# Performance work log

Measured on AMD Instinct MI355X. Metric: run time of the kernel, lower is better.

## Reference

```python
import jax, jax.numpy as jnp
import numpy as np

N, E = 50000, 800000
IN_DIM, HID, OUT = 512, 128, 64
EPS = 0.3
N_LAYERS = 2


def setup_inputs() -> dict:
    key = jax.random.key(0)
    ks = jax.random.split(key, 10)
    src = jax.random.randint(ks[0], (E,), 0, N, dtype=jnp.int32)
    dst = jax.random.randint(ks[1], (E,), 0, N, dtype=jnp.int32)
    yes_no = jax.random.randint(ks[2], (E,), 0, 2, dtype=jnp.int32)
    # symmetric degree norm d = (deg+1)^-1/2 (self-loop-adjusted, as in DGL FAGCN)
    deg = jax.ops.segment_sum(jnp.ones((E,), jnp.float32), dst, num_segments=N)
    d = jax.lax.rsqrt(deg + 1.0)
    return {
        "h": jax.random.normal(ks[3], (N, IN_DIM), jnp.float32),
        "d": d,
        "t1_w": jax.random.normal(ks[4], (HID, IN_DIM), jnp.float32) * (1.414 / np.sqrt(IN_DIM)),
        "t1_b": jnp.zeros((HID,), jnp.float32),
        "gate_w": jax.random.normal(ks[5], (N_LAYERS, 2 * HID), jnp.float32) * (1.414 / np.sqrt(2 * HID)),
        "gate_b": jnp.zeros((N_LAYERS,), jnp.float32),
        "t2_w": jax.random.normal(ks[6], (OUT, HID), jnp.float32) * (1.414 / np.sqrt(HID)),
        "t2_b": jnp.zeros((OUT,), jnp.float32),
        "yes_weight": jnp.float32(1.5),
        "no_weight": jnp.float32(-0.5),
        "src": src,
        "dst": dst,
        "yes_no": yes_no,
    }


def reference(h, d, t1_w, t1_b, gate_w, gate_b, t2_w, t2_b, yes_weight, no_weight, src, dst, yes_no):
    n = h.shape[0]
    hdim = t1_w.shape[0]
    yn = yes_no.astype(h.dtype)
    # yes/no edge bias is layer-independent
    yn_term = jnp.tanh(yn * yes_weight + (1.0 - yn) * no_weight)  # [E]
    dd = d[dst] * d[src]  # [E]

    x = jax.nn.relu(h @ t1_w.T + t1_b)  # [N, H] (dropout is identity in eval)
    raw = x
    for i in range(gate_w.shape[0]):
        # gate(concat(h_dst, h_src)) == h@w_dst (gathered at dst) + h@w_src (gathered at src)
        gd = x @ gate_w[i, :hdim]   # [N]
        gs = x @ gate_w[i, hdim:]   # [N]
        g = jnp.tanh(gd[dst] + gs[src] + gate_b[i])  # [E]
        e = (g + yn_term) * 0.5 * dd                 # [E]
        msg = x[src] * e[:, None]                    # [E, H]
        z = jax.ops.segment_sum(msg, dst, num_segments=n)  # [N, H]
        x = EPS * raw + z
    logits = x @ t2_w.T + t2_b
    return jax.nn.log_softmax(logits, axis=1)
```

## Files before the change

kernel.cpp:

```cpp
#include <hip/hip_runtime.h>
#include <math.h>

#define N_NODES 50000
#define N_EDGES 800000
#define IN_DIM  512
#define HID     128
#define OUT_DIM 64
#define EPS     0.3f

#define SCAN_BLOCKS 49
#define LDS_ROW 516

typedef __attribute__((ext_vector_type(8))) short bf16x8;
typedef __attribute__((ext_vector_type(8))) __bf16 bf16v8;
typedef __attribute__((ext_vector_type(4))) float f32x4;

__device__ __forceinline__ float fast_tanh(float x) {
    return 1.0f - 2.0f / (__expf(2.0f * x) + 1.0f);
}

__device__ __forceinline__ unsigned short f2bfu(float f) {
    return __builtin_bit_cast(unsigned short, (__bf16)f);
}
__device__ __forceinline__ unsigned pk2(float lo, float hi) {
    return (unsigned)f2bfu(lo) | ((unsigned)f2bfu(hi) << 16);
}
__device__ __forceinline__ float bf_lo(unsigned u) { return __uint_as_float(u << 16); }
__device__ __forceinline__ float bf_hi(unsigned u) { return __uint_as_float(u & 0xffff0000u); }

__device__ __forceinline__ int deg_of(float dv) {
    return (int)(1.0f / (dv * dv) + 0.5f) - 1;
}


__global__ void hw_k(const float* __restrict__ d, int* __restrict__ partials,
                     const float* __restrict__ w, unsigned short* __restrict__ wb) {
    int bid = blockIdx.x, tid = threadIdx.x;

    if (bid < SCAN_BLOCKS) {
        int base = bid * 1024 + tid * 4;
        int s = 0;
#pragma unroll
        for (int j = 0; j < 4; j++) if (base + j < N_NODES) s += deg_of(d[base + j]);
#pragma unroll
        for (int off = 32; off; off >>= 1) s += __shfl_down(s, off);
        __shared__ int ws[4];
        int lane = tid & 63, wv = tid >> 6;
        if (lane == 0) ws[wv] = s;
        __syncthreads();
        if (tid == 0) partials[bid] = ws[0] + ws[1] + ws[2] + ws[3];
        return;
    }

    int t = (bid - SCAN_BLOCKS) * 256 + tid;
    int lane = t & 63;
    int ct   = (t >> 6) & 7;
    int ks   = t >> 9;
    int row  = ct * 16 + (lane & 15);
    int kb   = ks * 32 + (lane >> 4) * 8;
    const float* p = &w[(size_t)row * IN_DIM + kb];
    float4 v0 = *(const float4*)p, v1 = *(const float4*)(p + 4);
    uint4 pk;
    pk.x = pk2(v0.x, v0.y);
    pk.y = pk2(v0.z, v0.w);
    pk.z = pk2(v1.x, v1.y);
    pk.w = pk2(v1.z, v1.w);
    *(uint4*)&wb[(size_t)t * 8] = pk;
}


__global__ void scanw_k(const float* __restrict__ d, const int* __restrict__ partials,
                        int* __restrict__ rowptr, int* __restrict__ cursor) {
    int tid = threadIdx.x;
    int base = blockIdx.x * 1024 + tid * 4;
    int v[4]; int s = 0;
#pragma unroll
    for (int j = 0; j < 4; j++) {
        v[j] = (base + j < N_NODES) ? deg_of(d[base + j]) : 0;
        s += v[j];
    }
    int lane = tid & 63, wv = tid >> 6;
    int sc = s;
#pragma unroll
    for (int off = 1; off < 64; off <<= 1) {
        int t = __shfl_up(sc, off);
        if (lane >= off) sc += t;
    }
    __shared__ int wtot[4];
    __shared__ int bofs_s;
    if (lane == 63) wtot[wv] = sc;
    if (tid < 64) {
        int p = (tid < blockIdx.x) ? partials[tid] : 0;
#pragma unroll
        for (int off = 32; off; off >>= 1) p += __shfl_down(p, off);
        if (tid == 0) bofs_s = p;
    }
    __syncthreads();
    int wof = 0;
    for (int w = 0; w < wv; w++) wof += wtot[w];
    int excl = bofs_s + wof + (sc - s);
#pragma unroll
    for (int j = 0; j < 4; j++) {
        if (base + j < N_NODES) { rowptr[base + j] = excl; cursor[base + j] = excl; }
        excl += v[j];
    }
    if (blockIdx.x == SCAN_BLOCKS - 1 && tid == 0)
        rowptr[N_NODES] = bofs_s + wtot[0] + wtot[1] + wtot[2] + wtot[3];
}


__launch_bounds__(256)
__global__ void t1fill_k(const float* __restrict__ h, const unsigned short* __restrict__ wb,
                         const float* __restrict__ bias, const float* __restrict__ gw0,
                         unsigned short* __restrict__ xb0,
                         float* __restrict__ gd0, float* __restrict__ gs0,
                         const int* __restrict__ src, const int* __restrict__ dst,
                         const int* __restrict__ yn, int* __restrict__ cursor,
                         int* __restrict__ csr) {
    __shared__ float At[16 * LDS_ROW];
    __shared__ float red[4][4][4][2];

    if (blockIdx.x & 1) {
        int e = (blockIdx.x >> 1) * 256 + threadIdx.x;
        int dv = dst[e];
        int pos = atomicAdd(&cursor[dv], 1);
        csr[pos] = src[e] | (yn[e] << 31);
        return;
    }

    int tid  = threadIdx.x;
    int lane = tid & 63;
    int wv   = tid >> 6;
    int l15  = lane & 15;
    int quad = lane >> 4;
    int rowb = (blockIdx.x >> 1) * 16;

#pragma unroll
    for (int i = 0; i < 8; ++i) {
        int c    = wv * 8 + i;
        int row  = c >> 1, half = c & 1;
        const float* gsrc = &h[(size_t)(rowb + row) * IN_DIM + half * 256 + lane * 4];
        float* ldst = &At[row * LDS_ROW + half * 256];
        __builtin_amdgcn_global_load_lds(
            (const __attribute__((address_space(1))) unsigned int*)gsrc,
            (__attribute__((address_space(3))) unsigned int*)ldst, 16, 0, 0);
    }
    __syncthreads();

    int ct0 = wv * 2;
    const unsigned short* bp = &wb[(size_t)lane * 8];
    const float* arp = &At[l15 * LDS_ROW + quad * 8];
    f32x4 acc[2];
    acc[0] = (f32x4){0.f, 0.f, 0.f, 0.f};
    acc[1] = (f32x4){0.f, 0.f, 0.f, 0.f};
#pragma unroll 4
    for (int ks = 0; ks < 16; ++ks) {
        float4 a0 = *(const float4*)(arp + ks * 32);
        float4 a1 = *(const float4*)(arp + ks * 32 + 4);
        bf16v8 av;
        av[0] = (__bf16)a0.x; av[1] = (__bf16)a0.y;
        av[2] = (__bf16)a0.z; av[3] = (__bf16)a0.w;
        av[4] = (__bf16)a1.x; av[5] = (__bf16)a1.y;
        av[6] = (__bf16)a1.z; av[7] = (__bf16)a1.w;
        bf16x8 af = __builtin_bit_cast(bf16x8, av);
        bf16x8 b0 = *(const bf16x8*)(bp + (size_t)(ks * 8 + ct0) * 512);
        bf16x8 b1 = *(const bf16x8*)(bp + (size_t)(ks * 8 + ct0 + 1) * 512);
        acc[0] = __builtin_amdgcn_mfma_f32_16x16x32_bf16(af, b0, acc[0], 0, 0, 0);
        acc[1] = __builtin_amdgcn_mfma_f32_16x16x32_bf16(af, b1, acc[1], 0, 0, 0);
    }

    float pd[4] = {0.f, 0.f, 0.f, 0.f}, ps[4] = {0.f, 0.f, 0.f, 0.f};
#pragma unroll
    for (int ct = 0; ct < 2; ++ct) {
        int o = (ct0 + ct) * 16 + l15;
        float b = bias[o];
        float wd = gw0[o], wsv = gw0[128 + o];
#pragma unroll
        for (int r = 0; r < 4; ++r) {
            float v = acc[ct][r] + b;
            v = v > 0.f ? v : 0.f;
            int node = rowb + quad * 4 + r;
            xb0[(size_t)node * HID + o] = f2bfu(v);
            pd[r] += v * wd; ps[r] += v * wsv;
        }
    }
#pragma unroll
    for (int m = 1; m < 16; m <<= 1) {
#pragma unroll
        for (int r = 0; r < 4; ++r) {
            pd[r] += __shfl_xor(pd[r], m);
            ps[r] += __shfl_xor(ps[r], m);
        }
    }
    if (l15 == 0) {
#pragma unroll
        for (int r = 0; r < 4; ++r) {
            red[wv][quad][r][0] = pd[r];
            red[wv][quad][r][1] = ps[r];
        }
    }
    __syncthreads();
    if (wv == 0 && lane < 16) {
        int q = lane >> 2, r = lane & 3;
        float sd = red[0][q][r][0] + red[1][q][r][0] + red[2][q][r][0] + red[3][q][r][0];
        float ss = red[0][q][r][1] + red[1][q][r][1] + red[2][q][r][1] + red[3][q][r][1];
        gd0[rowb + lane] = sd;
        gs0[rowb + lane] = ss;
    }
}


__global__ void agg_k(const unsigned short* __restrict__ xb,
                      const unsigned short* __restrict__ rb,
                      const int* __restrict__ rowptr, const int* __restrict__ csr,
                      const float* __restrict__ d,
                      const float* __restrict__ gd, const float* __restrict__ gs,
                      const float* __restrict__ gb, int layer,
                      const float* __restrict__ yw, const float* __restrict__ nw,
                      const float* __restrict__ gw_next,
                      float* __restrict__ gd_out, float* __restrict__ gs_out,
                      unsigned short* __restrict__ xb_out) {
    int t = blockIdx.x * blockDim.x + threadIdx.x;
    int nid = t >> 6, lane = t & 63;
    if (nid >= N_NODES) return;
    int l15 = lane & 15, eg = lane >> 4;
    float acc[8];
#pragma unroll
    for (int j = 0; j < 8; j++) acc[j] = 0.f;
    if (lane < 16) {
        uint4 rv = *(const uint4*)&rb[(size_t)nid * HID + l15 * 8];
        acc[0] = EPS * bf_lo(rv.x); acc[1] = EPS * bf_hi(rv.x);
        acc[2] = EPS * bf_lo(rv.y); acc[3] = EPS * bf_hi(rv.y);
        acc[4] = EPS * bf_lo(rv.z); acc[5] = EPS * bf_hi(rv.z);
        acc[6] = EPS * bf_lo(rv.w); acc[7] = EPS * bf_hi(rv.w);
    }
    float gdn = gd[nid] + gb[layer];
    float dn  = d[nid];
    float ty  = fast_tanh(yw[0]);
    float tno = fast_tanh(nw[0]);
    int e0 = rowptr[nid], e1 = rowptr[nid + 1];
    for (int b0 = e0; b0 < e1; b0 += 64) {
        int e = b0 + lane;
        float cf = 0.f; int sidx = 0;
        if (e < e1) {
            int p = csr[e];
            int s = p & 0x7fffffff;
            float ynt = (p < 0) ? ty : tno;
            cf = (fast_tanh(gdn + gs[s]) + ynt) * 0.5f * dn * d[s];
            sidx = s;
        }
        int trips = e1 - b0; if (trips > 64) trips = 64;
        float cfA = __shfl(cf, eg);
        int   sA  = __shfl(sidx, eg);
        uint4 vA  = *(const uint4*)&xb[(size_t)sA * HID + l15 * 8];
        for (int t4 = 0; t4 < trips; t4 += 4) {
            float cfB = 0.f; uint4 vB = make_uint4(0, 0, 0, 0);
            if (t4 + 4 < trips) {
                int nx = t4 + 4 + eg;
                cfB = __shfl(cf, nx);
                int sB = __shfl(sidx, nx);
                vB = *(const uint4*)&xb[(size_t)sB * HID + l15 * 8];
            }
            acc[0] += cfA * bf_lo(vA.x); acc[1] += cfA * bf_hi(vA.x);
            acc[2] += cfA * bf_lo(vA.y); acc[3] += cfA * bf_hi(vA.y);
            acc[4] += cfA * bf_lo(vA.z); acc[5] += cfA * bf_hi(vA.z);
            acc[6] += cfA * bf_lo(vA.w); acc[7] += cfA * bf_hi(vA.w);
            cfA = cfB; vA = vB;
        }
    }
#pragma unroll
    for (int j = 0; j < 8; j++) acc[j] += __shfl_xor(acc[j], 32);
#pragma unroll
    for (int j = 0; j < 8; j++) acc[j] += __shfl_xor(acc[j], 16);
    if (lane < 16) {
        uint4 pk;
        pk.x = pk2(acc[0], acc[1]);
        pk.y = pk2(acc[2], acc[3]);
        pk.z = pk2(acc[4], acc[5]);
        pk.w = pk2(acc[6], acc[7]);
        *(uint4*)&xb_out[(size_t)nid * HID + l15 * 8] = pk;
    }
    if (gw_next) {
        float pd = 0.f, psv = 0.f;
#pragma unroll
        for (int j = 0; j < 8; j++) {
            int o = l15 * 8 + j;
            pd  += acc[j] * gw_next[o];
            psv += acc[j] * gw_next[128 + o];
        }
#pragma unroll
        for (int m = 1; m < 16; m <<= 1) {
            pd  += __shfl_xor(pd, m);
            psv += __shfl_xor(psv, m);
        }
        if (lane == 0) { gd_out[nid] = pd; gs_out[nid] = psv; }
    }
}


__launch_bounds__(256)
__global__ void out_k(const unsigned short* __restrict__ xb, const float* __restrict__ w,
                      const float* __restrict__ bias, float* __restrict__ out) {
    __shared__ float As[64][132];
    __shared__ float Bs[64][132];
    int tid = threadIdx.x;
    int n0  = blockIdx.x * 64;
#pragma unroll
    for (int j = 0; j < 4; j++) {
        int c8 = tid + j * 256;
        int r = c8 >> 4, c = (c8 & 15) * 8;
        int gr = n0 + r;
        uint4 v = make_uint4(0, 0, 0, 0);
        if (gr < N_NODES) v = *(const uint4*)&xb[(size_t)gr * HID + c];
        *(float4*)&As[r][c]     = make_float4(bf_lo(v.x), bf_hi(v.x), bf_lo(v.y), bf_hi(v.y));
        *(float4*)&As[r][c + 4] = make_float4(bf_lo(v.z), bf_hi(v.z), bf_lo(v.w), bf_hi(v.w));
    }
#pragma unroll
    for (int j = 0; j < 8; j++) {
        int f4 = tid + j * 256;
        int r = f4 >> 5, c = (f4 & 31) * 4;
        *(float4*)&Bs[r][c] = *(const float4*)&w[r * HID + c];
    }
    __syncthreads();
    int tn = tid >> 4, to = tid & 15;
    float acc[4][4];
#pragma unroll
    for (int i = 0; i < 4; i++)
#pragma unroll
        for (int j = 0; j < 4; j++) acc[i][j] = 0.0f;
#pragma unroll 2
    for (int k = 0; k < HID; k += 4) {
        float4 av[4], bv[4];
#pragma unroll
        for (int i = 0; i < 4; i++) av[i] = *(const float4*)&As[tn + 16 * i][k];
#pragma unroll
        for (int j = 0; j < 4; j++) bv[j] = *(const float4*)&Bs[to + 16 * j][k];
#pragma unroll
        for (int i = 0; i < 4; i++)
#pragma unroll
            for (int j = 0; j < 4; j++) {
                acc[i][j] += av[i].x * bv[j].x;
                acc[i][j] += av[i].y * bv[j].y;
                acc[i][j] += av[i].z * bv[j].z;
                acc[i][j] += av[i].w * bv[j].w;
            }
    }
    float bj[4];
#pragma unroll
    for (int j = 0; j < 4; j++) bj[j] = bias[to + 16 * j];
#pragma unroll
    for (int i = 0; i < 4; i++) {
        float v[4];
        float m = -1e30f;
#pragma unroll
        for (int j = 0; j < 4; j++) { v[j] = acc[i][j] + bj[j]; m = fmaxf(m, v[j]); }
#pragma unroll
        for (int s = 1; s < 16; s <<= 1) m = fmaxf(m, __shfl_xor(m, s));
        float sum = 0.f;
#pragma unroll
        for (int j = 0; j < 4; j++) sum += __expf(v[j] - m);
#pragma unroll
        for (int s = 1; s < 16; s <<= 1) sum += __shfl_xor(sum, s);
        float lse = m + __logf(sum);
        int r = n0 + tn + 16 * i;
        if (r < N_NODES) {
#pragma unroll
            for (int j = 0; j < 4; j++) out[r * OUT_DIM + to + 16 * j] = v[j] - lse;
        }
    }
}


extern "C" void kernel_launch(void* const* d_in, const int* in_sizes, int n_in,
                              void* d_out, int out_size, void* d_ws, size_t ws_size,
                              hipStream_t stream) {
    const float* h    = (const float*)d_in[0];
    const float* d    = (const float*)d_in[1];
    const float* t1_w = (const float*)d_in[2];
    const float* t1_b = (const float*)d_in[3];
    const float* gw   = (const float*)d_in[4];
    const float* gb   = (const float*)d_in[5];
    const float* t2_w = (const float*)d_in[6];
    const float* t2_b = (const float*)d_in[7];
    const float* yw   = (const float*)d_in[8];
    const float* nw   = (const float*)d_in[9];
    const int* src    = (const int*)d_in[10];
    const int* dst    = (const int*)d_in[11];
    const int* yn     = (const int*)d_in[12];
    float* outp = (float*)d_out;

    char* ws = (char*)d_ws;
    size_t off = 0;
    auto alloc = [&](size_t bytes) {
        void* p = ws + off;
        off = (off + bytes + 255) & ~(size_t)255;
        return p;
    };
    unsigned short* xb0 = (unsigned short*)alloc((size_t)N_NODES * HID * 2);
    unsigned short* xb1 = (unsigned short*)alloc((size_t)N_NODES * HID * 2);
    unsigned short* xb2 = (unsigned short*)alloc((size_t)N_NODES * HID * 2);
    unsigned short* wb  = (unsigned short*)alloc((size_t)8192 * 8 * 2);
    float* gd0    = (float*)alloc((size_t)N_NODES * 4);
    float* gs0    = (float*)alloc((size_t)N_NODES * 4);
    float* gd1    = (float*)alloc((size_t)N_NODES * 4);
    float* gs1    = (float*)alloc((size_t)N_NODES * 4);
    int*   rowptr = (int*)alloc((size_t)(N_NODES + 1) * 4);
    int*   cursor = (int*)alloc((size_t)N_NODES * 4);
    int*   csr    = (int*)alloc((size_t)N_EDGES * 4);
    int*   partials = (int*)alloc(64 * 4);
    (void)ws_size; (void)n_in; (void)in_sizes; (void)out_size;

    hw_k<<<SCAN_BLOCKS + 32, 256, 0, stream>>>(d, partials, t1_w, wb);
    scanw_k<<<SCAN_BLOCKS, 256, 0, stream>>>(d, partials, rowptr, cursor);

    t1fill_k<<<2 * (N_NODES / 16), 256, 0, stream>>>(h, wb, t1_b, gw, xb0, gd0, gs0,
                                                     src, dst, yn, cursor, csr);

    int wave_blocks = (N_NODES * 64 + 255) / 256;

    agg_k<<<wave_blocks, 256, 0, stream>>>(xb0, xb0, rowptr, csr, d, gd0, gs0, gb, 0,
                                           yw, nw, gw + 256, gd1, gs1, xb1);
    agg_k<<<wave_blocks, 256, 0, stream>>>(xb1, xb0, rowptr, csr, d, gd1, gs1, gb, 1,
                                           yw, nw, (const float*)nullptr,
                                           (float*)nullptr, (float*)nullptr, xb2);

    out_k<<<(N_NODES + 63) / 64, 256, 0, stream>>>(xb2, t2_w, t2_b, outp);
}
```

Measured before the change: 330.7 us.

## Merge degree scan into one prep kernel and halve t1 LDS staging

Replaces the two-kernel partial-sum plus scan with a single prep kernel in which each scan block redundantly sums all preceding degrees, removing one launch and the partials buffer. The t1 GEMM now stages the h tile into LDS in two 256-column halves instead of the full 512 columns, halving the LDS footprint so more blocks can be resident per CU. The cost is redundant prefix reads of d in later scan blocks and an extra barrier pair per GEMM block.

```diff
diff --git a/kernel.cpp b/kernel.cpp
--- a/kernel.cpp
+++ b/kernel.cpp
@@ -9,7 +9,7 @@
 #define EPS     0.3f
 
 #define SCAN_BLOCKS 49
-#define LDS_ROW 516
+#define LDS_ROW_H 260
 
 typedef __attribute__((ext_vector_type(8))) short bf16x8;
 typedef __attribute__((ext_vector_type(8))) __bf16 bf16v8;
@@ -33,22 +33,51 @@
 }
 
 
-__global__ void hw_k(const float* __restrict__ d, int* __restrict__ partials,
-                     const float* __restrict__ w, unsigned short* __restrict__ wb) {
+__global__ void prep_k(const float* __restrict__ d,
+                       int* __restrict__ rowptr, int* __restrict__ cursor,
+                       const float* __restrict__ w, unsigned short* __restrict__ wb) {
     int bid = blockIdx.x, tid = threadIdx.x;
 
     if (bid < SCAN_BLOCKS) {
+        int lane = tid & 63, wv = tid >> 6;
+        __shared__ int wtot[4], wpre[4];
+        __shared__ int bofs_s;
+        int lim = bid * 1024;
+        int pre = 0;
+        for (int i = tid * 4; i < lim; i += 1024) {
+            float4 dv = *(const float4*)&d[i];
+            pre += deg_of(dv.x) + deg_of(dv.y) + deg_of(dv.z) + deg_of(dv.w);
+        }
+#pragma unroll
+        for (int off = 32; off; off >>= 1) pre += __shfl_down(pre, off);
+        if (lane == 0) wpre[wv] = pre;
         int base = bid * 1024 + tid * 4;
-        int s = 0;
-#pragma unroll
-        for (int j = 0; j < 4; j++) if (base + j < N_NODES) s += deg_of(d[base + j]);
-#pragma unroll
-        for (int off = 32; off; off >>= 1) s += __shfl_down(s, off);
-        __shared__ int ws[4];
-        int lane = tid & 63, wv = tid >> 6;
-        if (lane == 0) ws[wv] = s;
+        int v[4]; int s = 0;
+#pragma unroll
+        for (int j = 0; j < 4; j++) {
+            v[j] = (base + j < N_NODES) ? deg_of(d[base + j]) : 0;
+            s += v[j];
+        }
+        int sc = s;
+#pragma unroll
+        for (int off = 1; off < 64; off <<= 1) {
+            int t = __shfl_up(sc, off);
+            if (lane >= off) sc += t;
+        }
+        if (lane == 63) wtot[wv] = sc;
         __syncthreads();
-        if (tid == 0) partials[bid] = ws[0] + ws[1] + ws[2] + ws[3];
+        if (tid == 0) bofs_s = wpre[0] + wpre[1] + wpre[2] + wpre[3];
+        __syncthreads();
+        int wof = 0;
+        for (int w2 = 0; w2 < wv; w2++) wof += wtot[w2];
+        int excl = bofs_s + wof + (sc - s);
+#pragma unroll
+        for (int j = 0; j < 4; j++) {
+            if (base + j < N_NODES) { rowptr[base + j] = excl; cursor[base + j] = excl; }
+            excl += v[j];
+        }
+        if (bid == SCAN_BLOCKS - 1 && tid == 0)
+            rowptr[N_NODES] = bofs_s + wtot[0] + wtot[1] + wtot[2] + wtot[3];
         return;
     }
 
@@ -69,46 +98,6 @@
 }
 
 
-__global__ void scanw_k(const float* __restrict__ d, const int* __restrict__ partials,
-                        int* __restrict__ rowptr, int* __restrict__ cursor) {
-    int tid = threadIdx.x;
-    int base = blockIdx.x * 1024 + tid * 4;
-    int v[4]; int s = 0;
-#pragma unroll
-    for (int j = 0; j < 4; j++) {
-        v[j] = (base + j < N_NODES) ? deg_of(d[base + j]) : 0;
-        s += v[j];
-    }
-    int lane = tid & 63, wv = tid >> 6;
-    int sc = s;
-#pragma unroll
-    for (int off = 1; off < 64; off <<= 1) {
-        int t = __shfl_up(sc, off);
-        if (lane >= off) sc += t;
-    }
-    __shared__ int wtot[4];
-    __shared__ int bofs_s;
-    if (lane == 63) wtot[wv] = sc;
-    if (tid < 64) {
-        int p = (tid < blockIdx.x) ? partials[tid] : 0;
-#pragma unroll
-        for (int off = 32; off; off >>= 1) p += __shfl_down(p, off);
-        if (tid == 0) bofs_s = p;
-    }
-    __syncthreads();
-    int wof = 0;
-    for (int w = 0; w < wv; w++) wof += wtot[w];
-    int excl = bofs_s + wof + (sc - s);
-#pragma unroll
-    for (int j = 0; j < 4; j++) {
-        if (base + j < N_NODES) { rowptr[base + j] = excl; cursor[base + j] = excl; }
-        excl += v[j];
-    }
-    if (blockIdx.x == SCAN_BLOCKS - 1 && tid == 0)
-        rowptr[N_NODES] = bofs_s + wtot[0] + wtot[1] + wtot[2] + wtot[3];
-}
-
-
 __launch_bounds__(256)
 __global__ void t1fill_k(const float* __restrict__ h, const unsigned short* __restrict__ wb,
                          const float* __restrict__ bias, const float* __restrict__ gw0,
@@ -117,7 +106,7 @@
                          const int* __restrict__ src, const int* __restrict__ dst,
                          const int* __restrict__ yn, int* __restrict__ cursor,
                          int* __restrict__ csr) {
-    __shared__ float At[16 * LDS_ROW];
+    __shared__ float At[16 * LDS_ROW_H];
     __shared__ float red[4][4][4][2];
 
     if (blockIdx.x & 1) {
@@ -135,38 +124,43 @@
     int quad = lane >> 4;
     int rowb = (blockIdx.x >> 1) * 16;
 
-#pragma unroll
-    for (int i = 0; i < 8; ++i) {
-        int c    = wv * 8 + i;
-        int row  = c >> 1, half = c & 1;
-        const float* gsrc = &h[(size_t)(rowb + row) * IN_DIM + half * 256 + lane * 4];
-        float* ldst = &At[row * LDS_ROW + half * 256];
-        __builtin_amdgcn_global_load_lds(
-            (const __attribute__((address_space(1))) unsigned int*)gsrc,
-            (__attribute__((address_space(3))) unsigned int*)ldst, 16, 0, 0);
-    }
-    __syncthreads();
-
     int ct0 = wv * 2;
     const unsigned short* bp = &wb[(size_t)lane * 8];
-    const float* arp = &At[l15 * LDS_ROW + quad * 8];
+    const float* arp = &At[l15 * LDS_ROW_H + quad * 8];
     f32x4 acc[2];
     acc[0] = (f32x4){0.f, 0.f, 0.f, 0.f};
     acc[1] = (f32x4){0.f, 0.f, 0.f, 0.f};
+
+#pragma unroll
+    for (int ph = 0; ph < 2; ++ph) {
+#pragma unroll
+        for (int i = 0; i < 4; ++i) {
+            int row = wv * 4 + i;
+            const float* gsrc = &h[(size_t)(rowb + row) * IN_DIM + ph * 256 + lane * 4];
+            float* ldst = &At[row * LDS_ROW_H];
+            __builtin_amdgcn_global_load_lds(
+                (const __attribute__((address_space(1))) unsigned int*)gsrc,
+                (__attribute__((address_space(3))) unsigned int*)ldst, 16, 0, 0);
+        }
+        __syncthreads();
+
 #pragma unroll 4
-    for (int ks = 0; ks < 16; ++ks) {
-        float4 a0 = *(const float4*)(arp + ks * 32);
-        float4 a1 = *(const float4*)(arp + ks * 32 + 4);
-        bf16v8 av;
-        av[0] = (__bf16)a0.x; av[1] = (__bf16)a0.y;
-        av[2] = (__bf16)a0.z; av[3] = (__bf16)a0.w;
-        av[4] = (__bf16)a1.x; av[5] = (__bf16)a1.y;
-        av[6] = (__bf16)a1.z; av[7] = (__bf16)a1.w;
-        bf16x8 af = __builtin_bit_cast(bf16x8, av);
-        bf16x8 b0 = *(const bf16x8*)(bp + (size_t)(ks * 8 + ct0) * 512);
-        bf16x8 b1 = *(const bf16x8*)(bp + (size_t)(ks * 8 + ct0 + 1) * 512);
-        acc[0] = __builtin_amdgcn_mfma_f32_16x16x32_bf16(af, b0, acc[0], 0, 0, 0);
-        acc[1] = __builtin_amdgcn_mfma_f32_16x16x32_bf16(af, b1, acc[1], 0, 0, 0);
+        for (int ks = 0; ks < 8; ++ks) {
+            int ks_g = ph * 8 + ks;
+            float4 a0 = *(const float4*)(arp + ks * 32);
+            float4 a1 = *(const float4*)(arp + ks * 32 + 4);
+            bf16v8 av;
+            av[0] = (__bf16)a0.x; av[1] = (__bf16)a0.y;
+            av[2] = (__bf16)a0.z; av[3] = (__bf16)a0.w;
+            av[4] = (__bf16)a1.x; av[5] = (__bf16)a1.y;
+            av[6] = (__bf16)a1.z; av[7] = (__bf16)a1.w;
+            bf16x8 af = __builtin_bit_cast(bf16x8, av);
+            bf16x8 b0 = *(const bf16x8*)(bp + (size_t)(ks_g * 8 + ct0) * 512);
+            bf16x8 b1 = *(const bf16x8*)(bp + (size_t)(ks_g * 8 + ct0 + 1) * 512);
+            acc[0] = __builtin_amdgcn_mfma_f32_16x16x32_bf16(af, b0, acc[0], 0, 0, 0);
+            acc[1] = __builtin_amdgcn_mfma_f32_16x16x32_bf16(af, b1, acc[1], 0, 0, 0);
+        }
+        __syncthreads();
     }
 
     float pd[4] = {0.f, 0.f, 0.f, 0.f}, ps[4] = {0.f, 0.f, 0.f, 0.f};
@@ -407,11 +401,9 @@
     int*   rowptr = (int*)alloc((size_t)(N_NODES + 1) * 4);
     int*   cursor = (int*)alloc((size_t)N_NODES * 4);
     int*   csr    = (int*)alloc((size_t)N_EDGES * 4);
-    int*   partials = (int*)alloc(64 * 4);
     (void)ws_size; (void)n_in; (void)in_sizes; (void)out_size;
 
-    hw_k<<<SCAN_BLOCKS + 32, 256, 0, stream>>>(d, partials, t1_w, wb);
-    scanw_k<<<SCAN_BLOCKS, 256, 0, stream>>>(d, partials, rowptr, cursor);
+    prep_k<<<SCAN_BLOCKS + 32, 256, 0, stream>>>(d, rowptr, cursor, t1_w, wb);
 
     t1fill_k<<<2 * (N_NODES / 16), 256, 0, stream>>>(h, wb, t1_b, gw, xb0, gd0, gs0,
                                                      src, dst, yn, cursor, csr);
```

Measured after the change: 335.0 us. About the same (+1.3%).

## Halve t1 GEMM LDS tile with two-phase K loading and use nontemporal stores

Applied to the files above, without the earlier changes.

The t1fill kernel now stages the 16x512 input tile in two 256-column phases with a half-size LDS buffer, adding an extra barrier per phase. This roughly halves LDS usage per block so more blocks can be resident per CU. Separately, writes of intermediate features, gate scalars and CSR entries are switched to nontemporal stores to reduce cache pollution. The trade-off is extra synchronization and loss of load/compute overlap between phases. The nontemporal hint may also hurt, since several of these outputs are re-read by later kernels.

```diff
diff --git a/kernel.cpp b/kernel.cpp
--- a/kernel.cpp
+++ b/kernel.cpp
@@ -9,11 +9,12 @@
 #define EPS     0.3f
 
 #define SCAN_BLOCKS 49
-#define LDS_ROW 516
+#define LDS_ROW_H 260
 
 typedef __attribute__((ext_vector_type(8))) short bf16x8;
 typedef __attribute__((ext_vector_type(8))) __bf16 bf16v8;
 typedef __attribute__((ext_vector_type(4))) float f32x4;
+typedef __attribute__((ext_vector_type(4))) unsigned int u32x4;
 
 __device__ __forceinline__ float fast_tanh(float x) {
     return 1.0f - 2.0f / (__expf(2.0f * x) + 1.0f);
@@ -27,6 +28,10 @@
 }
 __device__ __forceinline__ float bf_lo(unsigned u) { return __uint_as_float(u << 16); }
 __device__ __forceinline__ float bf_hi(unsigned u) { return __uint_as_float(u & 0xffff0000u); }
+
+__device__ __forceinline__ void nt_store16(void* p, uint4 v) {
+    __builtin_nontemporal_store(__builtin_bit_cast(u32x4, v), (u32x4*)p);
+}
 
 __device__ __forceinline__ int deg_of(float dv) {
     return (int)(1.0f / (dv * dv) + 0.5f) - 1;
@@ -117,14 +122,14 @@
                          const int* __restrict__ src, const int* __restrict__ dst,
                          const int* __restrict__ yn, int* __restrict__ cursor,
                          int* __restrict__ csr) {
-    __shared__ float At[16 * LDS_ROW];
+    __shared__ float At[16 * LDS_ROW_H];
     __shared__ float red[4][4][4][2];
 
     if (blockIdx.x & 1) {
         int e = (blockIdx.x >> 1) * 256 + threadIdx.x;
         int dv = dst[e];
         int pos = atomicAdd(&cursor[dv], 1);
-        csr[pos] = src[e] | (yn[e] << 31);
+        __builtin_nontemporal_store(src[e] | (yn[e] << 31), &csr[pos]);
         return;
     }
 
@@ -135,38 +140,43 @@
     int quad = lane >> 4;
     int rowb = (blockIdx.x >> 1) * 16;
 
-#pragma unroll
-    for (int i = 0; i < 8; ++i) {
-        int c    = wv * 8 + i;
-        int row  = c >> 1, half = c & 1;
-        const float* gsrc = &h[(size_t)(rowb + row) * IN_DIM + half * 256 + lane * 4];
-        float* ldst = &At[row * LDS_ROW + half * 256];
-        __builtin_amdgcn_global_load_lds(
-            (const __attribute__((address_space(1))) unsigned int*)gsrc,
-            (__attribute__((address_space(3))) unsigned int*)ldst, 16, 0, 0);
-    }
-    __syncthreads();
-
     int ct0 = wv * 2;
     const unsigned short* bp = &wb[(size_t)lane * 8];
-    const float* arp = &At[l15 * LDS_ROW + quad * 8];
+    const float* arp = &At[l15 * LDS_ROW_H + quad * 8];
     f32x4 acc[2];
     acc[0] = (f32x4){0.f, 0.f, 0.f, 0.f};
     acc[1] = (f32x4){0.f, 0.f, 0.f, 0.f};
+
+#pragma unroll
+    for (int ph = 0; ph < 2; ++ph) {
+#pragma unroll
+        for (int i = 0; i < 4; ++i) {
+            int row = wv * 4 + i;
+            const float* gsrc = &h[(size_t)(rowb + row) * IN_DIM + ph * 256 + lane * 4];
+            float* ldst = &At[row * LDS_ROW_H];
+            __builtin_amdgcn_global_load_lds(
+                (const __attribute__((address_space(1))) unsigned int*)gsrc,
+                (__attribute__((address_space(3))) unsigned int*)ldst, 16, 0, 0);
+        }
+        __syncthreads();
+
 #pragma unroll 4
-    for (int ks = 0; ks < 16; ++ks) {
-        float4 a0 = *(const float4*)(arp + ks * 32);
-        float4 a1 = *(const float4*)(arp + ks * 32 + 4);
-        bf16v8 av;
-        av[0] = (__bf16)a0.x; av[1] = (__bf16)a0.y;
-        av[2] = (__bf16)a0.z; av[3] = (__bf16)a0.w;
-        av[4] = (__bf16)a1.x; av[5] = (__bf16)a1.y;
-        av[6] = (__bf16)a1.z; av[7] = (__bf16)a1.w;
-        bf16x8 af = __builtin_bit_cast(bf16x8, av);
-        bf16x8 b0 = *(const bf16x8*)(bp + (size_t)(ks * 8 + ct0) * 512);
-        bf16x8 b1 = *(const bf16x8*)(bp + (size_t)(ks * 8 + ct0 + 1) * 512);
-        acc[0] = __builtin_amdgcn_mfma_f32_16x16x32_bf16(af, b0, acc[0], 0, 0, 0);
-        acc[1] = __builtin_amdgcn_mfma_f32_16x16x32_bf16(af, b1, acc[1], 0, 0, 0);
+        for (int ks = 0; ks < 8; ++ks) {
+            int ks_g = ph * 8 + ks;
+            float4 a0 = *(const float4*)(arp + ks * 32);
+            float4 a1 = *(const float4*)(arp + ks * 32 + 4);
+            bf16v8 av;
+            av[0] = (__bf16)a0.x; av[1] = (__bf16)a0.y;
+            av[2] = (__bf16)a0.z; av[3] = (__bf16)a0.w;
+            av[4] = (__bf16)a1.x; av[5] = (__bf16)a1.y;
+            av[6] = (__bf16)a1.z; av[7] = (__bf16)a1.w;
+            bf16x8 af = __builtin_bit_cast(bf16x8, av);
+            bf16x8 b0 = *(const bf16x8*)(bp + (size_t)(ks_g * 8 + ct0) * 512);
+            bf16x8 b1 = *(const bf16x8*)(bp + (size_t)(ks_g * 8 + ct0 + 1) * 512);
+            acc[0] = __builtin_amdgcn_mfma_f32_16x16x32_bf16(af, b0, acc[0], 0, 0, 0);
+            acc[1] = __builtin_amdgcn_mfma_f32_16x16x32_bf16(af, b1, acc[1], 0, 0, 0);
+        }
+        __syncthreads();
     }
 
     float pd[4] = {0.f, 0.f, 0.f, 0.f}, ps[4] = {0.f, 0.f, 0.f, 0.f};
@@ -180,7 +190,7 @@
             float v = acc[ct][r] + b;
             v = v > 0.f ? v : 0.f;
             int node = rowb + quad * 4 + r;
-            xb0[(size_t)node * HID + o] = f2bfu(v);
+            __builtin_nontemporal_store(f2bfu(v), &xb0[(size_t)node * HID + o]);
             pd[r] += v * wd; ps[r] += v * wsv;
         }
     }
@@ -204,8 +214,8 @@
         int q = lane >> 2, r = lane & 3;
         float sd = red[0][q][r][0] + red[1][q][r][0] + red[2][q][r][0] + red[3][q][r][0];
         float ss = red[0][q][r][1] + red[1][q][r][1] + red[2][q][r][1] + red[3][q][r][1];
-        gd0[rowb + lane] = sd;
-        gs0[rowb + lane] = ss;
+        __builtin_nontemporal_store(sd, &gd0[rowb + lane]);
+        __builtin_nontemporal_store(ss, &gs0[rowb + lane]);
     }
 }
 
@@ -278,7 +288,7 @@
         pk.y = pk2(acc[2], acc[3]);
         pk.z = pk2(acc[4], acc[5]);
         pk.w = pk2(acc[6], acc[7]);
-        *(uint4*)&xb_out[(size_t)nid * HID + l15 * 8] = pk;
+        nt_store16(&xb_out[(size_t)nid * HID + l15 * 8], pk);
     }
     if (gw_next) {
         float pd = 0.f, psv = 0.f;
@@ -293,7 +303,10 @@
             pd  += __shfl_xor(pd, m);
             psv += __shfl_xor(psv, m);
         }
-        if (lane == 0) { gd_out[nid] = pd; gs_out[nid] = psv; }
+        if (lane == 0) {
+            __builtin_nontemporal_store(pd, &gd_out[nid]);
+            __builtin_nontemporal_store(psv, &gs_out[nid]);
+        }
     }
 }
 
```

Result: no change. 336.4 us (+1.7%).
